# Kernel optimization log

Measured on AMD Instinct MI355X. Metric: run time of the kernel, lower is better.

## Reference

```python
import jax, jax.numpy as jnp
import numpy as np

N, E = 50000, 800000
IN_C, EDGE_IN, HID, HEADS = 16, 16, 32, 4


def setup_inputs() -> dict:
    key = jax.random.key(0)
    ks = jax.random.split(key, 16)
    HC = HEADS * HID
    def lin(k, fan_in, shape):
        b = 1.0 / np.sqrt(fan_in)
        return jax.random.uniform(k, shape, jnp.float32, -b, b)
    return {
        "x": jax.random.normal(ks[0], (N, IN_C), jnp.float32),
        "edge_index": jax.random.randint(ks[1], (2, E), 0, N, jnp.int64),
        "edge_attr": jax.random.normal(ks[2], (E, EDGE_IN), jnp.float32),
        # TransformerConv params
        "Wq": lin(ks[3], IN_C, (IN_C, HC)), "bq": lin(ks[4], IN_C, (HC,)),
        "Wk": lin(ks[5], IN_C, (IN_C, HC)), "bk": lin(ks[6], IN_C, (HC,)),
        "Wv": lin(ks[7], IN_C, (IN_C, HC)), "bv": lin(ks[8], IN_C, (HC,)),
        "We": lin(ks[9], EDGE_IN, (EDGE_IN, HC)),  # lin_edge has no bias in PyG
        "Wskip": lin(ks[10], IN_C, (IN_C, HID)), "bskip": lin(ks[11], IN_C, (HID,)),
        # edge MLP params
        "W1": lin(ks[12], 2 * HID + EDGE_IN, (2 * HID + EDGE_IN, HID)),
        "b1": lin(ks[13], 2 * HID + EDGE_IN, (HID,)),
        "W2": lin(ks[14], HID, (HID, 1)), "b2": lin(ks[15], HID, (1,)),
    }


def _forward(x, edge_attr, Wq, bq, Wk, bk, Wv, bv, We, Wskip, bskip, W1, b1, W2, b2, src, dst):
    n = x.shape[0]
    q = (x @ Wq + bq).reshape(n, HEADS, HID)
    k = (x @ Wk + bk).reshape(n, HEADS, HID)
    v = (x @ Wv + bv).reshape(n, HEADS, HID)
    e = (edge_attr @ We).reshape(-1, HEADS, HID)  # [E,H,C]
    kj = k[src] + e                               # key of source node + edge emb
    alpha = jnp.einsum('ehc,ehc->eh', q[dst], kj) / jnp.sqrt(jnp.float32(HID))
    # segment softmax over incoming edges of each dst node (per head)
    m = jax.ops.segment_max(alpha, dst, num_segments=n)      # [N,H]
    a = jnp.exp(alpha - m[dst])
    s = jax.ops.segment_sum(a, dst, num_segments=n)          # [N,H]
    a = a / s[dst]
    msg = (v[src] + e) * a[:, :, None]                        # [E,H,C]
    out = jax.ops.segment_sum(msg, dst, num_segments=n)      # [N,H,C]
    out = out.mean(axis=1)                                    # concat=False -> mean over heads
    out = out + x @ Wskip + bskip                              # root/skip connection
    # edge MLP on gather-concat features
    feat = jnp.concatenate([out[src], edge_attr, out[dst]], axis=-1)
    h = jax.nn.relu(feat @ W1 + b1)
    return (h @ W2 + b2).reshape(-1)


def reference(x, edge_index, edge_attr, Wq, bq, Wk, bk, Wv, bv, We, Wskip, bskip, W1, b1, W2, b2):
    src, dst = edge_index[0], edge_index[1]
    return _forward(x, edge_attr, Wq, bq, Wk, bk, Wv, bv, We, Wskip, bskip, W1, b1, W2, b2, src, dst)
```

## Files before the change

kernel.cpp:

```cpp
#include <hip/hip_runtime.h>
#include <hip/hip_fp16.h>

#define NN 50000
#define NE 800000
#define NB 196
#define EPB 3125
#define NODE_BLOCKS 12500

#define SL 0.25506413f

#define PMV 0
#define MEV 1024
#define BEV 2048
#define UPV 2112
#define WPV 2176
#define WCV 2240
#define P_TOTAL 2304

template <int CTRL>
__device__ __forceinline__ float dpp_add(float v) {
  int m = __builtin_amdgcn_update_dpp(0, __builtin_bit_cast(int, v), CTRL, 0xF, 0xF, true);
  return v + __builtin_bit_cast(float, m);
}
__device__ __forceinline__ float row16_reduce(float v) {
  v = dpp_add<0xB1>(v);
  v = dpp_add<0x4E>(v);
  v = dpp_add<0x124>(v);
  v = dpp_add<0x128>(v);
  return v;
}

__global__ __launch_bounds__(256) void precompute_kernel(
    const float* __restrict__ Wq, const float* __restrict__ Wk,
    const float* __restrict__ bq, const float* __restrict__ bk,
    const float* __restrict__ We, float* __restrict__ P) {
  int t = threadIdx.x;
  for (int idx = t; idx < 1024; idx += 256) {
    int lane = idx >> 4, i = idx & 15;
    int h = lane >> 4, tt = lane & 15;
    float am = 0.f, ae = 0.f;
#pragma unroll
    for (int c = 0; c < 32; c++) {
      float wq = Wq[i * 128 + h * 32 + c];
      am += wq * Wk[tt * 128 + h * 32 + c];
      ae += wq * We[tt * 128 + h * 32 + c];
    }
    P[PMV + idx] = am * SL;
    P[MEV + idx] = ae * SL;
  }
  if (t < 64) {
    int h = t >> 4, tt = t & 15;
    float be = 0.f, up = 0.f, wp = 0.f;
#pragma unroll
    for (int c = 0; c < 32; c++) {
      be += bq[h * 32 + c] * We[tt * 128 + h * 32 + c];
      up += Wq[tt * 128 + h * 32 + c] * bk[h * 32 + c];
      wp += bq[h * 32 + c] * Wk[tt * 128 + h * 32 + c];
    }
    P[BEV + t] = be * SL;
    P[UPV + t] = up * SL;
    P[WPV + t] = wp * SL;
  }
  if (t < 4) {
    float wc = 0.f;
#pragma unroll
    for (int c = 0; c < 32; c++) wc += bq[t * 32 + c] * bk[t * 32 + c];
    P[WCV + t] = wc * SL;
  }
}

__global__ __launch_bounds__(256) void node_linear_kernel(
    const float* __restrict__ x, const float* __restrict__ P,
    const int* __restrict__ ei, int* __restrict__ hist_all,
    float* __restrict__ y, float* __restrict__ qe,
    float* __restrict__ u4) {
  __shared__ int hist[NB];
  if (blockIdx.x >= NODE_BLOCKS) {
    int b = blockIdx.x - NODE_BLOCKS;
    int t = threadIdx.x;
    if (t < NB) hist[t] = 0;
    __syncthreads();
    int base = b * EPB;
    for (int i = t; i < EPB; i += 256)
      atomicAdd(&hist[ei[NE + base + i] >> 8], 1);
    __syncthreads();
    if (t < NB) hist_all[t * 256 + b] = hist[t];
    return;
  }
  int wave = threadIdx.x >> 6;
  int lane = threadIdx.x & 63;
  int n = blockIdx.x * 4 + wave;
  int h = lane >> 4, t = lane & 15;

  const float4* xp = (const float4*)(x + n * 16);
  float4 X0 = xp[0], X1 = xp[1], X2 = xp[2], X3 = xp[3];
  float xr[16] = {X0.x, X0.y, X0.z, X0.w, X1.x, X1.y, X1.z, X1.w,
                  X2.x, X2.y, X2.z, X2.w, X3.x, X3.y, X3.z, X3.w};

  const float4* pm = (const float4*)(P + PMV) + lane * 4;
  const float4* me = (const float4*)(P + MEV) + lane * 4;
  float yt = 0.f, qv = P[BEV + lane];
#pragma unroll
  for (int i4 = 0; i4 < 4; i4++) {
    float4 m = pm[i4], e = me[i4];
    yt += xr[4 * i4] * m.x + xr[4 * i4 + 1] * m.y
        + xr[4 * i4 + 2] * m.z + xr[4 * i4 + 3] * m.w;
    qv += xr[4 * i4] * e.x + xr[4 * i4 + 1] * e.y
        + xr[4 * i4 + 2] * e.z + xr[4 * i4 + 3] * e.w;
  }
  y[n * 64 + lane] = yt;
  qe[n * 64 + lane] = qv;

  float pu = P[UPV + lane] * xr[t];
  pu = row16_reduce(pu);
  if (t == 0) u4[n * 4 + h] = pu;
}

__global__ __launch_bounds__(256) void scan_buckets_kernel(
    int* __restrict__ hist_all, int* __restrict__ btot) {
  int wv = blockIdx.x * 4 + (threadIdx.x >> 6);
  int l = threadIdx.x & 63;
  if (wv >= NB) return;
  int base = wv * 256;
  int run = 0;
#pragma unroll
  for (int c = 0; c < 4; c++) {
    int v = hist_all[base + c * 64 + l];
    int orig = v;
#pragma unroll
    for (int d = 1; d < 64; d <<= 1) {
      int u = __shfl_up(v, d);
      if (l >= d) v += u;
    }
    hist_all[base + c * 64 + l] = run + v - orig;
    run += __shfl(v, 63);
  }
  if (l == 0) btot[wv] = run;
}

__global__ __launch_bounds__(256) void tiny_scan_kernel(
    const int* __restrict__ btot, int* __restrict__ coarse_offs) {
  __shared__ int sc[256];
  int t = threadIdx.x;
  int v = (t < NB) ? btot[t] : 0;
  sc[t] = v;
  __syncthreads();
  for (int d = 1; d < 256; d <<= 1) {
    int u = (t >= d) ? sc[t - d] : 0;
    __syncthreads();
    sc[t] += u;
    __syncthreads();
  }
  if (t < NB) coarse_offs[t] = sc[t] - v;
  if (t == NB - 1) coarse_offs[NB] = sc[t];
}

__global__ __launch_bounds__(256) void bucket_scatter_kernel(
    const int* __restrict__ ei, const int* __restrict__ cursor_all,
    const int* __restrict__ coarse_offs, int2* __restrict__ s_tmp) {
  __shared__ int cur[NB];
  int t = threadIdx.x, b = blockIdx.x;
  if (t < NB) cur[t] = cursor_all[t * 256 + b] + coarse_offs[t];
  __syncthreads();
  int base = b * EPB;
  for (int i = t; i < EPB; i += 256) {
    int e = base + i;
    int src = ei[e], dst = ei[NE + e];
    int pos = atomicAdd(&cur[dst >> 8], 1);
    s_tmp[pos] = make_int2(src | ((dst & 255) << 16), e);
  }
}

__global__ __launch_bounds__(256) void fine_csr_kernel(
    const int2* __restrict__ s_tmp, const int* __restrict__ coarse_offs,
    int2* __restrict__ s_se, int* __restrict__ csrpos,
    int* __restrict__ offs) {
  __shared__ int cnt[256], sc[256], cur[256];
  int t = threadIdx.x, b = blockIdx.x;
  int lo = coarse_offs[b], hi = coarse_offs[b + 1];
  cnt[t] = 0;
  __syncthreads();
  for (int p = lo + t; p < hi; p += 256)
    atomicAdd(&cnt[(s_tmp[p].x >> 16) & 255], 1);
  __syncthreads();
  int myc = cnt[t];
  sc[t] = myc;
  __syncthreads();
  for (int d = 1; d < 256; d <<= 1) {
    int v = (t >= d) ? sc[t - d] : 0;
    __syncthreads();
    sc[t] += v;
    __syncthreads();
  }
  int excl = sc[t] - myc;
  cur[t] = lo + excl;
  int gd = b * 256 + t;
  if (gd <= NN) offs[gd] = lo + excl;
  __syncthreads();
  for (int p = lo + t; p < hi; p += 256) {
    int2 m = s_tmp[p];
    int pos = atomicAdd(&cur[(m.x >> 16) & 255], 1);
    s_se[pos] = make_int2(m.x & 0xFFFF, m.y);
    csrpos[m.y] = pos;
  }
}

__global__ __launch_bounds__(256) void ea_place_kernel(
    const float* __restrict__ edge_attr, const int* __restrict__ csrpos,
    uint4* __restrict__ s_ea4) {
  int e = blockIdx.x * 256 + threadIdx.x;
  const float4* eap = (const float4*)(edge_attr + (size_t)e * 16);
  float4 a = eap[0], bb = eap[1], c = eap[2], d = eap[3];
  uint4 u0, u1;
  __half2 hh;
  hh = __floats2half2_rn(a.x, a.y);   u0.x = *(unsigned*)&hh;
  hh = __floats2half2_rn(a.z, a.w);   u0.y = *(unsigned*)&hh;
  hh = __floats2half2_rn(bb.x, bb.y); u0.z = *(unsigned*)&hh;
  hh = __floats2half2_rn(bb.z, bb.w); u0.w = *(unsigned*)&hh;
  hh = __floats2half2_rn(c.x, c.y);   u1.x = *(unsigned*)&hh;
  hh = __floats2half2_rn(c.z, c.w);   u1.y = *(unsigned*)&hh;
  hh = __floats2half2_rn(d.x, d.y);   u1.z = *(unsigned*)&hh;
  hh = __floats2half2_rn(d.z, d.w);   u1.w = *(unsigned*)&hh;
  int pos = csrpos[e];
  s_ea4[(size_t)pos * 2]     = u0;
  s_ea4[(size_t)pos * 2 + 1] = u1;
}

__global__ __launch_bounds__(256) void aggregate_kernel(
    const float* __restrict__ y, const float* __restrict__ qe,
    const float* __restrict__ u4,
    const float* __restrict__ x, const __half* __restrict__ s_ea,
    const int2* __restrict__ s_se, const float* __restrict__ P,
    const float* __restrict__ We, const float* __restrict__ Wv,
    const float* __restrict__ bv,
    const float* __restrict__ Wskip, const float* __restrict__ bskip,
    const float* __restrict__ W1, const float* __restrict__ b1,
    const int* __restrict__ offs,
    __half* __restrict__ Ah, __half* __restrict__ Cbh) {
  int wave = threadIdx.x >> 6, lane = threadIdx.x & 63;
  int n = blockIdx.x * 4 + wave;
  int h = lane >> 4, t = lane & 15;
  int base = h * 32 + t;
  int gb = lane & 48;

  float yt2 = y[n * 64 + lane] + P[WPV + lane];
  float qet = qe[n * 64 + lane];
  float un_wc = u4[n * 4 + h] + P[WCV + h];
  int off = offs[n], end = offs[n + 1];

  float s = 0.f, ax = 0.f, ae = 0.f;
  int j = off;
  for (; j + 8 <= end; j += 8) {
    const uint4* sp = (const uint4*)&s_se[j];
    uint4 sa = sp[0], sb = sp[1], sc4 = sp[2], sd = sp[3];
    int src[8] = {(int)sa.x, (int)sa.z, (int)sb.x, (int)sb.z,
                  (int)sc4.x, (int)sc4.z, (int)sd.x, (int)sd.z};
    float xs[8], ea[8];
#pragma unroll
    for (int u = 0; u < 8; u++) {
      xs[u] = x[(unsigned)src[u] * 16u + (unsigned)t];
      ea[u] = __half2float(s_ea[(size_t)(j + u) * 16 + t]);
    }
    float p[8];
#pragma unroll
    for (int u = 0; u < 8; u++) p[u] = fmaf(yt2, xs[u], qet * ea[u]);
#pragma unroll
    for (int u = 0; u < 8; u++) p[u] = row16_reduce(p[u]);
#pragma unroll
    for (int u = 0; u < 8; u++) {
      float wgt = exp2f(p[u] + un_wc);
      s += wgt;
      ax = fmaf(wgt, xs[u], ax);
      ae = fmaf(wgt, ea[u], ae);
    }
  }
  for (; j < end; j++) {
    int srcu = s_se[j].x;
    float xs = x[(unsigned)srcu * 16u + (unsigned)t];
    float ea_ = __half2float(s_ea[(size_t)j * 16 + t]);
    float p = fmaf(yt2, xs, qet * ea_);
    p = row16_reduce(p);
    float wgt = exp2f(p + un_wc);
    s += wgt;
    ax = fmaf(wgt, xs, ax);
    ae = fmaf(wgt, ea_, ae);
  }

  float inv = (end > off) ? 1.f / s : 0.f;
  float dflag = (end > off) ? 1.f : 0.f;
  float axn = ax * inv, aen = ae * inv;
  float r0 = dflag * bv[base], r1 = dflag * bv[base + 16];
#pragma unroll
  for (int i = 0; i < 16; i++) {
    float axi = __shfl(axn, gb | i);
    float aei = __shfl(aen, gb | i);
    r0 += axi * Wv[i * 128 + base]      + aei * We[i * 128 + base];
    r1 += axi * Wv[i * 128 + base + 16] + aei * We[i * 128 + base + 16];
  }
  r0 += __shfl_xor(r0, 16); r0 += __shfl_xor(r0, 32);
  r1 += __shfl_xor(r1, 16); r1 += __shfl_xor(r1, 32);

  float sk0 = bskip[t], sk1 = bskip[t + 16];
#pragma unroll
  for (int i = 0; i < 16; i++) {
    float xi = x[n * 16 + i];
    sk0 += xi * Wskip[i * 32 + t];
    sk1 += xi * Wskip[i * 32 + t + 16];
  }
  float o0 = 0.25f * r0 + sk0;
  float o1 = 0.25f * r1 + sk1;

  int jj = lane & 31;
  int roff = (lane < 32) ? 0 : 48;
  float acc = (lane < 32) ? 0.f : b1[jj];
#pragma unroll
  for (int i = 0; i < 16; i++) {
    float oi = __shfl(o0, i);
    acc += oi * W1[(roff + i) * 32 + jj];
  }
#pragma unroll
  for (int i = 0; i < 16; i++) {
    float oi = __shfl(o1, i);
    acc += oi * W1[(roff + 16 + i) * 32 + jj];
  }
  float nb = __shfl_xor(acc, 1);
  if ((lane & 1) == 0) {
    __half2 hh = __floats2half2_rn(acc, nb);
    if (lane < 32) *(__half2*)(Ah  + n * 32 + jj) = hh;
    else           *(__half2*)(Cbh + n * 32 + jj) = hh;
  }
}

__global__ __launch_bounds__(256) void mlp_kernel(
    const int2* __restrict__ s_se, const __half* __restrict__ s_ea,
    const int* __restrict__ offs,
    const __half* __restrict__ Ah, const __half* __restrict__ Cbh,
    const float* __restrict__ W1, const float* __restrict__ W2,
    const float* __restrict__ b2v, float* __restrict__ out) {
  int wave = threadIdx.x >> 6, lane = threadIdx.x & 63;
  int n = blockIdx.x * 4 + wave;
  int g = lane >> 5, l = lane & 31;

  float w1e[16];
#pragma unroll
  for (int i = 0; i < 16; i++) w1e[i] = W1[(32 + i) * 32 + l];
  float w2j = W2[l];
  float b2s = b2v[0];
  float cb = __half2float(Cbh[n * 32 + l]);
  int off = offs[n], end = offs[n + 1];

  int p = off + g;
  for (; p + 2 < end; p += 4) {
    int2 se0 = s_se[p];
    int2 se1 = s_se[p + 2];
    float a0 = __half2float(Ah[(unsigned)se0.x * 32u + l]);
    float a1 = __half2float(Ah[(unsigned)se1.x * 32u + l]);
    const uint4* e0p = (const uint4*)(s_ea + (size_t)p * 16);
    const uint4* e1p = (const uint4*)(s_ea + (size_t)(p + 2) * 16);
    uint4 u00 = e0p[0], u01 = e0p[1];
    uint4 u10 = e1p[0], u11 = e1p[1];
    float h0 = a0 + cb, h1 = a1 + cb;
    const __half2* q00 = (const __half2*)&u00;
    const __half2* q01 = (const __half2*)&u01;
    const __half2* q10 = (const __half2*)&u10;
    const __half2* q11 = (const __half2*)&u11;
#pragma unroll
    for (int i = 0; i < 4; i++) {
      float2 f;
      f = __half22float2(q00[i]); h0 += f.x * w1e[2*i]   + f.y * w1e[2*i+1];
      f = __half22float2(q01[i]); h0 += f.x * w1e[8+2*i] + f.y * w1e[8+2*i+1];
      f = __half22float2(q10[i]); h1 += f.x * w1e[2*i]   + f.y * w1e[2*i+1];
      f = __half22float2(q11[i]); h1 += f.x * w1e[8+2*i] + f.y * w1e[8+2*i+1];
    }
    float v0 = fmaxf(h0, 0.f) * w2j;
    float v1 = fmaxf(h1, 0.f) * w2j;
    v0 = row16_reduce(v0); v1 = row16_reduce(v1);
    v0 += __shfl_xor(v0, 16); v1 += __shfl_xor(v1, 16);
    if (l == 0) {
      out[se0.y] = v0 + b2s;
      out[se1.y] = v1 + b2s;
    }
  }
  if (p < end) {
    int2 se = s_se[p];
    float a = __half2float(Ah[(unsigned)se.x * 32u + l]);
    const uint4* eap = (const uint4*)(s_ea + (size_t)p * 16);
    uint4 u0 = eap[0], u1 = eap[1];
    float hsum = a + cb;
    const __half2* hp0 = (const __half2*)&u0;
    const __half2* hp1 = (const __half2*)&u1;
#pragma unroll
    for (int i = 0; i < 4; i++) {
      float2 f0 = __half22float2(hp0[i]);
      hsum += f0.x * w1e[2 * i] + f0.y * w1e[2 * i + 1];
      float2 f1 = __half22float2(hp1[i]);
      hsum += f1.x * w1e[8 + 2 * i] + f1.y * w1e[8 + 2 * i + 1];
    }
    float hv = fmaxf(hsum, 0.f) * w2j;
    hv = row16_reduce(hv);
    hv += __shfl_xor(hv, 16);
    if (l == 0) out[se.y] = hv + b2s;
  }
}

extern "C" void kernel_launch(void* const* d_in, const int* in_sizes, int n_in,
                              void* d_out, int out_size, void* d_ws, size_t ws_size,
                              hipStream_t stream) {
  const float* x         = (const float*)d_in[0];
  const int*   ei        = (const int*)d_in[1];
  const float* edge_attr = (const float*)d_in[2];
  const float* Wq = (const float*)d_in[3],  *bq = (const float*)d_in[4];
  const float* Wk = (const float*)d_in[5],  *bk = (const float*)d_in[6];
  const float* Wv = (const float*)d_in[7],  *bv = (const float*)d_in[8];
  const float* We = (const float*)d_in[9];
  const float* Wskip = (const float*)d_in[10], *bskip = (const float*)d_in[11];
  const float* W1 = (const float*)d_in[12], *b1 = (const float*)d_in[13];
  const float* W2 = (const float*)d_in[14], *b2 = (const float*)d_in[15];
  float* out = (float*)d_out;

  char* w = (char*)d_ws;
  float*   y    = (float*)w;            w += (size_t)NN * 64 * 4;
  float*   qe   = (float*)w;            w += (size_t)NN * 64 * 4;
  float*   u4   = (float*)w;            w += (size_t)NN * 4 * 4;
  int2*    s_se = (int2*)w;             w += (size_t)NE * 8;
  int2*    s_tmp = (int2*)w;
  __half*  Ah   = (__half*)s_tmp;
  __half*  Cbh  = (__half*)((char*)s_tmp + (size_t)NN * 32 * 2);
  w += (size_t)NE * 8;
  uint4*   s_ea4 = (uint4*)w;           w += (size_t)NE * 32;
  int*     csrpos = (int*)w;            w += (size_t)NE * 4;
  int*     hist_all = (int*)w;          w += (size_t)256 * 256 * 4;
  int*     btot = (int*)w;              w += 256 * 4;
  int*     coarse_offs = (int*)w;       w += 256 * 4;
  int*     offs = (int*)w;              w += ((size_t)NN + 1) * 4;
  float*   P    = (float*)w;            w += (size_t)P_TOTAL * 4;

  precompute_kernel<<<1, 256, 0, stream>>>(Wq, Wk, bq, bk, We, P);
  node_linear_kernel<<<NODE_BLOCKS + 256, 256, 0, stream>>>(
      x, P, ei, hist_all, y, qe, u4);
  scan_buckets_kernel<<<49, 256, 0, stream>>>(hist_all, btot);
  tiny_scan_kernel<<<1, 256, 0, stream>>>(btot, coarse_offs);
  bucket_scatter_kernel<<<256, 256, 0, stream>>>(ei, hist_all, coarse_offs,
                                                 s_tmp);
  fine_csr_kernel<<<NB, 256, 0, stream>>>(s_tmp, coarse_offs, s_se, csrpos,
                                          offs);
  ea_place_kernel<<<NE / 256, 256, 0, stream>>>(edge_attr, csrpos, s_ea4);
  aggregate_kernel<<<NN / 4, 256, 0, stream>>>(y, qe, u4, x,
                                               (const __half*)s_ea4, s_se, P,
                                               We, Wv, bv, Wskip, bskip, W1, b1,
                                               offs, Ah, Cbh);
  mlp_kernel<<<NN / 4, 256, 0, stream>>>(s_se, (const __half*)s_ea4, offs,
                                         Ah, Cbh, W1, W2, b2, out);
}
```

Measured before the change: 229.3 us.

## Split edge histogram/scatter into more blocks and use LDS broadcast in aggregate

The edge histogram and bucket scatter now use 800 blocks of 1000 edges each instead of 256 blocks of 3125, so more CUs stay busy. The bucket scan is generalised to handle the wider per-bucket rows. Separately, the aggregate kernel now broadcasts its normalized vectors through shared memory with float4 reads, replacing the per-element cross-lane shuffles. The cost is a larger histogram array, a longer scan, and shared-memory traffic in the aggregate kernel.

```diff
diff --git a/kernel.cpp b/kernel.cpp
--- a/kernel.cpp
+++ b/kernel.cpp
@@ -4,7 +4,8 @@
 #define NN 50000
 #define NE 800000
 #define NB 196
-#define EPB 3125
+#define HB 800
+#define EPB 1000
 #define NODE_BLOCKS 12500
 
 #define SL 0.25506413f
@@ -84,7 +85,7 @@
     for (int i = t; i < EPB; i += 256)
       atomicAdd(&hist[ei[NE + base + i] >> 8], 1);
     __syncthreads();
-    if (t < NB) hist_all[t * 256 + b] = hist[t];
+    if (t < NB) hist_all[t * HB + b] = hist[t];
     return;
   }
   int wave = threadIdx.x >> 6;
@@ -121,18 +122,19 @@
   int wv = blockIdx.x * 4 + (threadIdx.x >> 6);
   int l = threadIdx.x & 63;
   if (wv >= NB) return;
-  int base = wv * 256;
+  int base = wv * HB;
   int run = 0;
 #pragma unroll
-  for (int c = 0; c < 4; c++) {
-    int v = hist_all[base + c * 64 + l];
+  for (int c = 0; c < (HB + 63) / 64; c++) {
+    int idx = c * 64 + l;
+    int v = (idx < HB) ? hist_all[base + idx] : 0;
     int orig = v;
 #pragma unroll
     for (int d = 1; d < 64; d <<= 1) {
       int u = __shfl_up(v, d);
       if (l >= d) v += u;
     }
-    hist_all[base + c * 64 + l] = run + v - orig;
+    if (idx < HB) hist_all[base + idx] = run + v - orig;
     run += __shfl(v, 63);
   }
   if (l == 0) btot[wv] = run;
@@ -160,7 +162,7 @@
     const int* __restrict__ coarse_offs, int2* __restrict__ s_tmp) {
   __shared__ int cur[NB];
   int t = threadIdx.x, b = blockIdx.x;
-  if (t < NB) cur[t] = cursor_all[t * 256 + b] + coarse_offs[t];
+  if (t < NB) cur[t] = cursor_all[t * HB + b] + coarse_offs[t];
   __syncthreads();
   int base = b * EPB;
   for (int i = t; i < EPB; i += 256) {
@@ -237,11 +239,11 @@
     const float* __restrict__ W1, const float* __restrict__ b1,
     const int* __restrict__ offs,
     __half* __restrict__ Ah, __half* __restrict__ Cbh) {
+  __shared__ float red[4][128];
   int wave = threadIdx.x >> 6, lane = threadIdx.x & 63;
   int n = blockIdx.x * 4 + wave;
   int h = lane >> 4, t = lane & 15;
   int base = h * 32 + t;
-  int gb = lane & 48;
 
   float yt2 = y[n * 64 + lane] + P[WPV + lane];
   float qet = qe[n * 64 + lane];
@@ -288,14 +290,25 @@
 
   float inv = (end > off) ? 1.f / s : 0.f;
   float dflag = (end > off) ? 1.f : 0.f;
-  float axn = ax * inv, aen = ae * inv;
+  float* rw = red[wave];
+  rw[lane] = ax * inv;
+  rw[64 + lane] = ae * inv;
+
   float r0 = dflag * bv[base], r1 = dflag * bv[base + 16];
-#pragma unroll
-  for (int i = 0; i < 16; i++) {
-    float axi = __shfl(axn, gb | i);
-    float aei = __shfl(aen, gb | i);
-    r0 += axi * Wv[i * 128 + base]      + aei * We[i * 128 + base];
-    r1 += axi * Wv[i * 128 + base + 16] + aei * We[i * 128 + base + 16];
+  const float4* axp = (const float4*)&rw[h * 16];
+  const float4* aep = (const float4*)&rw[64 + h * 16];
+#pragma unroll
+  for (int k = 0; k < 4; k++) {
+    float4 a4 = axp[k], e4 = aep[k];
+    int i0 = 4 * k;
+    r0 += a4.x * Wv[(i0    ) * 128 + base] + e4.x * We[(i0    ) * 128 + base];
+    r0 += a4.y * Wv[(i0 + 1) * 128 + base] + e4.y * We[(i0 + 1) * 128 + base];
+    r0 += a4.z * Wv[(i0 + 2) * 128 + base] + e4.z * We[(i0 + 2) * 128 + base];
+    r0 += a4.w * Wv[(i0 + 3) * 128 + base] + e4.w * We[(i0 + 3) * 128 + base];
+    r1 += a4.x * Wv[(i0    ) * 128 + base + 16] + e4.x * We[(i0    ) * 128 + base + 16];
+    r1 += a4.y * Wv[(i0 + 1) * 128 + base + 16] + e4.y * We[(i0 + 1) * 128 + base + 16];
+    r1 += a4.z * Wv[(i0 + 2) * 128 + base + 16] + e4.z * We[(i0 + 2) * 128 + base + 16];
+    r1 += a4.w * Wv[(i0 + 3) * 128 + base + 16] + e4.w * We[(i0 + 3) * 128 + base + 16];
   }
   r0 += __shfl_xor(r0, 16); r0 += __shfl_xor(r0, 32);
   r1 += __shfl_xor(r1, 16); r1 += __shfl_xor(r1, 32);
@@ -310,18 +323,28 @@
   float o0 = 0.25f * r0 + sk0;
   float o1 = 0.25f * r1 + sk1;
 
+  if (lane < 16) {
+    rw[t] = o0;
+    rw[16 + t] = o1;
+  }
+
   int jj = lane & 31;
   int roff = (lane < 32) ? 0 : 48;
   float acc = (lane < 32) ? 0.f : b1[jj];
-#pragma unroll
-  for (int i = 0; i < 16; i++) {
-    float oi = __shfl(o0, i);
-    acc += oi * W1[(roff + i) * 32 + jj];
-  }
-#pragma unroll
-  for (int i = 0; i < 16; i++) {
-    float oi = __shfl(o1, i);
-    acc += oi * W1[(roff + 16 + i) * 32 + jj];
+  const float4* op = (const float4*)rw;
+#pragma unroll
+  for (int k = 0; k < 4; k++) {
+    float4 o4 = op[k];
+    int r = roff + 4 * k;
+    acc += o4.x * W1[(r    ) * 32 + jj] + o4.y * W1[(r + 1) * 32 + jj]
+         + o4.z * W1[(r + 2) * 32 + jj] + o4.w * W1[(r + 3) * 32 + jj];
+  }
+#pragma unroll
+  for (int k = 0; k < 4; k++) {
+    float4 o4 = op[4 + k];
+    int r = roff + 16 + 4 * k;
+    acc += o4.x * W1[(r    ) * 32 + jj] + o4.y * W1[(r + 1) * 32 + jj]
+         + o4.z * W1[(r + 2) * 32 + jj] + o4.w * W1[(r + 3) * 32 + jj];
   }
   float nb = __shfl_xor(acc, 1);
   if ((lane & 1) == 0) {
@@ -429,19 +452,19 @@
   w += (size_t)NE * 8;
   uint4*   s_ea4 = (uint4*)w;           w += (size_t)NE * 32;
   int*     csrpos = (int*)w;            w += (size_t)NE * 4;
-  int*     hist_all = (int*)w;          w += (size_t)256 * 256 * 4;
+  int*     hist_all = (int*)w;          w += (size_t)NB * HB * 4;
   int*     btot = (int*)w;              w += 256 * 4;
   int*     coarse_offs = (int*)w;       w += 256 * 4;
   int*     offs = (int*)w;              w += ((size_t)NN + 1) * 4;
   float*   P    = (float*)w;            w += (size_t)P_TOTAL * 4;
 
   precompute_kernel<<<1, 256, 0, stream>>>(Wq, Wk, bq, bk, We, P);
-  node_linear_kernel<<<NODE_BLOCKS + 256, 256, 0, stream>>>(
+  node_linear_kernel<<<NODE_BLOCKS + HB, 256, 0, stream>>>(
       x, P, ei, hist_all, y, qe, u4);
   scan_buckets_kernel<<<49, 256, 0, stream>>>(hist_all, btot);
   tiny_scan_kernel<<<1, 256, 0, stream>>>(btot, coarse_offs);
-  bucket_scatter_kernel<<<256, 256, 0, stream>>>(ei, hist_all, coarse_offs,
-                                                 s_tmp);
+  bucket_scatter_kernel<<<HB, 256, 0, stream>>>(ei, hist_all, coarse_offs,
+                                                s_tmp);
   fine_csr_kernel<<<NB, 256, 0, stream>>>(s_tmp, coarse_offs, s_se, csrpos,
                                           offs);
   ea_place_kernel<<<NE / 256, 256, 0, stream>>>(edge_attr, csrpos, s_ea4);
```

Measured after the change: 227.8 us. About the same (-0.7%).
